# Kernel optimization log

Hardware: AMD Instinct MI355X
Metric: run time of the kernel (lower is better)

## Reference

```python
import jax, jax.numpy as jnp
import numpy as np

# Config (mirrors CorrLayerDownsample(J=3, L=8, A=1, A_prime=1, M=256, N=256,
# num_channels=1, shift_mode='samec', mask_angles=4)). With samec + 1 channel,
# every pair is 'shifted' (mask index 1) and groups (j1,j2) are contiguous in
# the global moment order, so concatenation reproduces results_storage order.
J, L, A, M, N, NB = 3, 8, 1, 256, 256, 2
MASK_ANGLES = 4
RADII = (1, 2)  # dyadic shift radii (assumed form of create_masks_shift)

def _mask_positions():
    # shift mask 1: origin plus shifts along mask_angles directions at dyadic radii
    pos = {(0, 0)}
    for k in range(MASK_ANGLES):
        th = np.pi * k / MASK_ANGLES
        for r in RADII:
            pos.add((int(round(r * np.cos(th))), int(round(r * np.sin(th)))))
    return sorted(pos)

def _union_flat_idx(h, w):
    # row-major flat indices of the union shift mask at resolution (h, w),
    # matching torch boolean-mask indexing order (mask_downsample + mask_idx_map_1)
    return np.array(sorted(((dx % h) * w + (dy % w)) for dx, dy in _mask_positions()), dtype=np.int64)

UNION_IDX = [_union_flat_idx(M >> j, N >> j) for j in range(J)]
NSHIFT = len(UNION_IDX[0])

# per-(j1,j2) channel gather indices: la = A*L*c + A*l + a = l (A=1, c=0)
# loop order in compute_idx: l1 outer, l2 inner
LA1 = np.repeat(np.arange(L), L)
LA2 = np.tile(np.arange(L), L)

def _spectral_pad(xh, Mn, Nn):
    # zero-pad Fourier representation to (Mn, Nn) -- spectral upsampling
    m, n = xh.shape[-2], xh.shape[-1]
    if (m, n) == (Mn, Nn):
        return xh
    xs = jnp.fft.fftshift(xh, axes=(-2, -1))
    ph, pw = (Mn - m) // 2, (Nn - n) // 2
    pad = [(0, 0)] * (xh.ndim - 2) + [(ph, ph), (pw, pw)]
    xp = jnp.pad(xs, pad)
    return jnp.fft.ifftshift(xp, axes=(-2, -1)) * ((Mn * Nn) / (m * n))

def _forward(xpsi_0, xpsi_1, xpsi_2):
    xs = [xpsi_0, xpsi_1, xpsi_2]
    hats = [jnp.fft.fft2(x.astype(jnp.complex64)) for x in xs]  # [nb, C, h_j, w_j]
    la1 = jnp.asarray(LA1)
    la2 = jnp.asarray(LA2)
    outs = []
    for j1 in range(J):
        h, w = M >> j1, N >> j1
        uidx = jnp.asarray(UNION_IDX[j1])
        h1 = hats[j1][:, la1]  # [nb, P=L*L, h, w]
        for j2 in range(j1, J):
            h2 = hats[j2][:, la2]
            if j2 > j1:
                h2 = _spectral_pad(h2, h, w)  # upsample coarser scale to scale j1
            corr = jnp.fft.ifft2(h1 * jnp.conj(h2)).real  # cross-correlation map
            flat = corr.reshape(corr.shape[0], corr.shape[1], h * w)
            outs.append(flat[:, :, uidx])  # masked downsample: keep shift positions
    return jnp.concatenate(outs, axis=1)  # [nb, total_pairs, NSHIFT]

def setup_inputs():
    key = jax.random.key(0)
    ks = jax.random.split(key, 3)
    return {
        "xpsi_0": jax.random.normal(ks[0], (NB, A * L, M, N), dtype=jnp.float32),
        "xpsi_1": jax.random.normal(ks[1], (NB, A * L, M // 2, N // 2), dtype=jnp.float32),
        "xpsi_2": jax.random.normal(ks[2], (NB, A * L, M // 4, N // 4), dtype=jnp.float32),
    }

def reference(xpsi_0, xpsi_1, xpsi_2):
    return _forward(xpsi_0, xpsi_1, xpsi_2)
```

## Files before the change

### kernel.cpp

```cpp
#include <hip/hip_runtime.h>

#define PI_D 3.14159265358979323846
#define PI_F 3.14159265358979323846f


__device__ inline float rtab_val(int n, int m2, int t) {
  if (t == 0) return 1.0f;
  double th = PI_D * (double)t / (double)n;
  double v = sin(th * (double)(m2 - 1)) / sin(th) + cos(th * (double)m2);
  return (float)(v / (double)m2);
}

__global__ __launch_bounds__(256) void k_front(
    const float* __restrict__ X0, const float* __restrict__ X1,
    const float* __restrict__ X2, float* __restrict__ P1p,
    float* __restrict__ P2p, float* __restrict__ V01, float* __restrict__ V02,
    float* __restrict__ V12, float* __restrict__ T01, float* __restrict__ T02,
    float* __restrict__ T12, float* __restrict__ out) {
  __shared__ float fsm[2304];
  int bid = blockIdx.x;
  int t = threadIdx.x;
  if (bid == 512) {
    for (int i = t; i < 5376; i += 256) out[i] = 0.f;
    return;
  }
  if (bid < 192) {
    const float* X; float* P; int lg, nsp, idx0;
    if (bid < 128) { X = X1; P = P1p; lg = 7; nsp = 8; idx0 = bid; }
    else           { X = X2; P = P2p; lg = 6; nsp = 4; idx0 = bid - 128; }
    int ch = idx0 / nsp, split = idx0 % nsp;
    int n = 1 << lg;
    int total = n * n;
    int chunk = total / nsp;
    int b0 = split * chunk;
    const float* x = X + (size_t)ch * total + b0;
    float s = 0.f;
    for (int i = t; i < chunk; i += 256) {
      int idx = b0 + i;
      float v = x[i];
      s += (((idx >> lg) ^ idx) & 1) ? -v : v;
    }
#pragma unroll
    for (int off = 32; off > 0; off >>= 1) s += __shfl_down(s, off, 64);
    __shared__ float red[4];
    if ((t & 63) == 0) red[t >> 6] = s;
    __syncthreads();
    if (t == 0) P[ch * nsp + split] = red[0] + red[1] + red[2] + red[3];
    return;
  }
  if (bid < 320) {
    int idx = bid - 192;
    int ch = idx >> 3, nxg = (idx & 7) * 16;
    float* Rl = fsm;
    float* Xs = fsm + 256;
    for (int i = t; i < 256; i += 256) Rl[i] = rtab_val(256, 128, i);
    const float4* xch4 =
        (const float4*)(X1 + (size_t)ch * 16384 + (size_t)nxg * 128);
    for (int i = t; i < 512; i += 256) ((float4*)Xs)[i] = xch4[i];
    __syncthreads();
    if (idx == 0)
      for (int i = t; i < 256; i += 256) T01[i] = Rl[i];
    float* vch = V01 + (size_t)ch * 128 * 256;
    for (int i = t; i < 2048; i += 256) {
      int r = i >> 7, k = i & 127;
      vch[(size_t)(nxg + r) * 256 + 2 * k] = Xs[r * 128 + k];
    }
    int cid = t & 63, wq = t >> 6;
    int m0 = 2 * cid + 1, m1 = 2 * cid + 129;
    float acc[4][2];
#pragma unroll
    for (int r = 0; r < 4; ++r) { acc[r][0] = 0.f; acc[r][1] = 0.f; }
    for (int ny = 0; ny < 128; ++ny) {
      float r0 = Rl[(m0 - 2 * ny) & 255];
      float r1 = Rl[(m1 - 2 * ny) & 255];
#pragma unroll
      for (int r = 0; r < 4; ++r) {
        float xv = Xs[(4 * wq + r) * 128 + ny];
        acc[r][0] += xv * r0;
        acc[r][1] += xv * r1;
      }
    }
#pragma unroll
    for (int r = 0; r < 4; ++r) {
      vch[(size_t)(nxg + 4 * wq + r) * 256 + m0] = acc[r][0];
      vch[(size_t)(nxg + 4 * wq + r) * 256 + m1] = acc[r][1];
    }
    return;
  }
  {
    int vbid = bid - 320;
    const float* X = X2; float* V;
    int n1, n2, s, ch, nxg, colh;
    if (vbid < 128) {
      V = V02; n1 = 256; n2 = 64; s = 4;
      ch = vbid >> 3; nxg = ((vbid >> 1) & 3) * 16; colh = vbid & 1;
    } else {
      int w = vbid - 128;
      V = V12; n1 = 128; n2 = 64; s = 2;
      ch = w >> 2; nxg = (w & 3) * 16; colh = 0;
    }
    float* Rl = fsm;
    float* Xs = fsm + 256;
    for (int i = t; i < n1; i += 256) Rl[i] = rtab_val(n1, n2, i);
    const float4* xch4 =
        (const float4*)(X + (size_t)ch * n2 * n2 + (size_t)nxg * n2);
    int nx4 = (16 * n2) >> 2;
    for (int i = t; i < nx4; i += 256) ((float4*)Xs)[i] = xch4[i];
    __syncthreads();
    if (vbid == 0)
      for (int i = t; i < 256; i += 256) T02[i] = Rl[i];
    if (vbid == 128)
      for (int i = t; i < 128; i += 256) T12[i] = Rl[i];
    int myq = (t & 63) + colh * 128;
    int nxq = t >> 6;
    int mask = n1 - 1;
    float acc[4][2];
#pragma unroll
    for (int r = 0; r < 4; ++r)
#pragma unroll
      for (int c = 0; c < 2; ++c) acc[r][c] = 0.f;
    for (int ny = 0; ny < n2; ++ny) {
      float xv[4];
#pragma unroll
      for (int r = 0; r < 4; ++r) xv[r] = Xs[(4 * nxq + r) * n2 + ny];
#pragma unroll
      for (int c = 0; c < 2; ++c) {
        float rv = Rl[(myq + 64 * c - s * ny) & mask];
#pragma unroll
        for (int r = 0; r < 4; ++r) acc[r][c] += xv[r] * rv;
      }
    }
    float* vch = V + (size_t)ch * n2 * n1;
#pragma unroll
    for (int r = 0; r < 4; ++r)
      for (int c = 0; c < 2; ++c)
        vch[(size_t)(nxg + 4 * nxq + r) * n1 + myq + 64 * c] = acc[r][c];
  }
}

__global__ __launch_bounds__(256) void k_main(const float* __restrict__ X0,
                                              const float* __restrict__ X1,
                                              const float* __restrict__ X2,
                                              const float* __restrict__ V01,
                                              const float* __restrict__ V02,
                                              const float* __restrict__ V12,
                                              const float* __restrict__ P1p,
                                              const float* __restrict__ P2p,
                                              const float* __restrict__ T01,
                                              const float* __restrict__ T02,
                                              const float* __restrict__ T12,
                                              float* __restrict__ out) {
  __shared__ float sRl[256];
  __shared__ float sh[4864];
  __shared__ float Vs[2][1024];
  int u = blockIdx.x;
  int t = threadIdx.x;
  int lane = t & 63;
  int wv = t >> 6;

  int b, l2, base, lgn1, mxg;
  const float* A1b;

  if (u < 640) {
    const float* V; const float* Pp; const float* T;
    int n1, n2, s, ch, chunk, nsp; float inv;
    if (u < 256) {
      V = V01; Pp = P1p; nsp = 8; A1b = X0; n1 = 256; n2 = 128; s = 2;
      inv = 1.f / 16384.f; ch = u >> 4; chunk = u & 15; lgn1 = 8; base = 64;
      T = T01;
    } else if (u < 512) {
      int w = u - 256;
      V = V02; Pp = P2p; nsp = 4; A1b = X0; n1 = 256; n2 = 64; s = 4;
      inv = 1.f / 4096.f; ch = w >> 4; chunk = w & 15; lgn1 = 8; base = 128;
      T = T02;
    } else {
      int w = u - 512;
      V = V12; Pp = P2p; nsp = 4; A1b = X1; n1 = 128; n2 = 64; s = 2;
      inv = 1.f / 4096.f; ch = w >> 3; chunk = w & 7; lgn1 = 7; base = 256;
      T = T12;
    }
    int mask = n1 - 1;
    for (int i = t; i < n1; i += 256) sRl[i] = T[i];
    mxg = chunk * 16;
    b = ch >> 3; l2 = ch & 7;
    const float* vch = V + (size_t)ch * n2 * n1;
    float Pv = 0.f;
    for (int i = 0; i < nsp; ++i) Pv += Pp[ch * nsp + i];
    float a = PI_F / (float)s;
    int per = 2 * s;

    if (n1 == 256) {
      if (s == 2) {
        for (int i = t; i < 640; i += 256) {
          int rl = 2 * (i >> 6), c4 = (i & 63) * 4;
          int mx = (mxg - 2 + rl) & 255;
          *(float4*)&sh[rl * 256 + c4] =
              *(const float4*)(vch + (size_t)(mx >> 1) * 256 + c4);
        }
      } else {
        for (int i = t; i < 320; i += 256) {
          int rl = 2 + 4 * (i >> 6), c4 = (i & 63) * 4;
          int mx = (mxg - 2 + rl) & 255;
          *(float4*)&sh[rl * 256 + c4] =
              *(const float4*)(vch + (size_t)(mx >> 2) * 256 + c4);
        }
      }
    } else {
      for (int i = t; i < 320; i += 256) {
        int rl = 2 * (i >> 5), c4 = (i & 31) * 4;
        int mx = (mxg - 2 + rl) & 127;
        *(float4*)&sh[rl * 128 + c4] =
            *(const float4*)(vch + (size_t)(mx >> 1) * 128 + c4);
      }
    }

    int nr, rls[4];
    if (s == 2) {
      if (wv == 0)      { nr = 3; rls[0] = 1;  rls[1] = 3;  rls[2] = 5;  rls[3] = 1; }
      else if (wv == 1) { nr = 2; rls[0] = 7;  rls[1] = 9;  rls[2] = 7;  rls[3] = 7; }
      else if (wv == 2) { nr = 2; rls[0] = 11; rls[1] = 13; rls[2] = 11; rls[3] = 11; }
      else              { nr = 2; rls[0] = 15; rls[1] = 17; rls[2] = 15; rls[3] = 15; }
    } else {
      if (wv == 0)      { nr = 4; rls[0] = 0;  rls[1] = 1;  rls[2] = 3;  rls[3] = 4; }
      else if (wv == 1) { nr = 4; rls[0] = 5;  rls[1] = 7;  rls[2] = 8;  rls[3] = 9; }
      else if (wv == 2) { nr = 3; rls[0] = 11; rls[1] = 12; rls[2] = 13; rls[3] = 11; }
      else              { nr = 3; rls[0] = 15; rls[1] = 16; rls[2] = 17; rls[3] = 15; }
    }
    int bj[4];
#pragma unroll
    for (int j = 0; j < 4; ++j) bj[j] = (mxg - 2 + rls[j]) & mask;

    const float4* vp4 = (const float4*)vch;
    if (n1 == 256) {
      int ntl = n2 >> 2;
      ((float4*)Vs[0])[t] = vp4[t];
      __syncthreads();
      float4 acc[4];
#pragma unroll
      for (int j = 0; j < 4; ++j) acc[j] = make_float4(0.f, 0.f, 0.f, 0.f);
      for (int tl = 0; tl < ntl; ++tl) {
        float4 stg;
        bool has = (tl + 1 < ntl);
        if (has) stg = vp4[(size_t)(tl + 1) * 256 + t];
        const float* Vc = Vs[tl & 1];
#pragma unroll
        for (int kk = 0; kk < 4; ++kk) {
          float4 vv = *(const float4*)&Vc[kk * 256 + 4 * lane];
          int ss = s * (4 * tl + kk);
#pragma unroll
          for (int j = 0; j < 4; ++j)
            if (j < nr) {
              float rv = sRl[(bj[j] - ss) & 255];
              acc[j].x += rv * vv.x;
              acc[j].y += rv * vv.y;
              acc[j].z += rv * vv.z;
              acc[j].w += rv * vv.w;
            }
        }
        if (has) ((float4*)Vs[(tl & 1) ^ 1])[t] = stg;
        __syncthreads();
      }
      float smy[4];
#pragma unroll
      for (int j = 0; j < 4; ++j)
        smy[j] = sinf(a * (float)((4 * lane + j) & (per - 1)));
#pragma unroll
      for (int j = 0; j < 4; ++j)
        if (j < nr) {
          float q = inv * sinf(a * (float)(bj[j] & (per - 1))) * Pv;
          float4 o = acc[j];
          o.x -= q * smy[0];
          o.y -= q * smy[1];
          o.z -= q * smy[2];
          o.w -= q * smy[3];
          *(float4*)&sh[rls[j] * 256 + 4 * lane] = o;
        }
    } else {
      if (t < 128) ((float4*)Vs[0])[t] = vp4[t];
      __syncthreads();
      float2 acc[4];
#pragma unroll
      for (int j = 0; j < 4; ++j) acc[j] = make_float2(0.f, 0.f);
      for (int tl = 0; tl < 16; ++tl) {
        float4 stg;
        bool has = (tl + 1 < 16) && (t < 128);
        if (has) stg = vp4[(size_t)(tl + 1) * 128 + t];
        const float* Vc = Vs[tl & 1];
#pragma unroll
        for (int kk = 0; kk < 4; ++kk) {
          float2 vv = *(const float2*)&Vc[kk * 128 + 2 * lane];
          int ss = 2 * (4 * tl + kk);
#pragma unroll
          for (int j = 0; j < 4; ++j)
            if (j < nr) {
              float rv = sRl[(bj[j] - ss) & 127];
              acc[j].x += rv * vv.x;
              acc[j].y += rv * vv.y;
            }
        }
        if (has) ((float4*)Vs[(tl & 1) ^ 1])[t] = stg;
        __syncthreads();
      }
      const float a2 = PI_F * 0.5f;
      float smy0 = sinf(a2 * (float)((2 * lane) & 3));
      float smy1 = sinf(a2 * (float)((2 * lane + 1) & 3));
#pragma unroll
      for (int j = 0; j < 4; ++j)
        if (j < nr) {
          float q = inv * sinf(a2 * (float)(bj[j] & 3)) * Pv;
          float2 o = acc[j];
          o.x -= q * smy0;
          o.y -= q * smy1;
          *(float2*)&sh[rls[j] * 128 + 2 * lane] = o;
        }
    }
  } else {
    int w = u - 640;
    const float* Ab; int loc, lgc;
    if (w < 256)      { loc = w;       Ab = X0; lgn1 = 8; lgc = 4; base = 0;   }
    else if (w < 384) { loc = w - 256; Ab = X1; lgn1 = 7; lgc = 3; base = 192; }
    else              { loc = w - 384; Ab = X2; lgn1 = 6; lgc = 2; base = 320; }
    int n1 = 1 << lgn1;
    int mask = n1 - 1;
    int n1sq = n1 * n1;
    int chunk = loc & ((1 << lgc) - 1);
    int bl2 = loc >> lgc;
    b = bl2 >> 3; l2 = bl2 & 7;
    A1b = Ab;
    const float* A2 = Ab + (size_t)(b * 8 + l2) * n1sq;
    mxg = chunk * 16;
    int nst = (19 * n1) >> 2;
    int l2n1 = lgn1 - 2;
    for (int i = t; i < nst; i += 256) {
      int rl = i >> l2n1;
      int c4 = (i & ((n1 >> 2) - 1)) * 4;
      int src = (mxg - 2 + rl) & mask;
      *(float4*)&sh[rl * n1 + c4] = *(const float4*)(A2 + (size_t)src * n1 + c4);
    }
  }
  __syncthreads();

  float accC[8][7];
#pragma unroll
  for (int i = 0; i < 8; ++i)
#pragma unroll
    for (int p = 0; p < 7; ++p) accC[i][p] = 0.f;
  {
    int n1 = 1 << lgn1;
    int mask = n1 - 1;
    int n1sq = n1 * n1;
    int lgtpr = lgn1 - 2;
    int tpr = 1 << lgtpr;
    int rif = 256 >> lgtpr;
    int rid = t >> lgtpr;
    int cid2 = t & (tpr - 1);
    int ty = cid2 * 4;
    int tym = (ty - 4) & mask;
    const float* A1 = A1b + (size_t)(b * 8) * n1sq;
    for (int rr = 0; rr < 16; rr += rif) {
      int ri = rr + rid;
      const float* r0 = &sh[(ri + 2) * n1];
      const float* r1 = &sh[(ri + 1) * n1];
      const float* r2 = &sh[ri * n1];
      const float* r3 = &sh[(ri + 3) * n1];
      float4 a0 = *(const float4*)(r0 + tym);
      float4 b0 = *(const float4*)(r0 + ty);
      float4 a1 = *(const float4*)(r1 + tym);
      float4 b1 = *(const float4*)(r1 + ty);
      float4 b2 = *(const float4*)(r2 + ty);
      float4 a3 = *(const float4*)(r3 + tym);
      float4 b3 = *(const float4*)(r3 + ty);
      const float* rA = A1 + (size_t)(mxg + ri) * n1 + ty;
#pragma unroll
      for (int l1 = 0; l1 < 8; ++l1) {
        float4 xv = *(const float4*)(rA + (size_t)l1 * n1sq);
        accC[l1][0] += xv.x * b0.x + xv.y * b0.y + xv.z * b0.z + xv.w * b0.w;
        accC[l1][1] += xv.x * a0.w + xv.y * b0.x + xv.z * b0.y + xv.w * b0.z;
        accC[l1][2] += xv.x * a0.z + xv.y * a0.w + xv.z * b0.x + xv.w * b0.y;
        accC[l1][3] += xv.x * b1.x + xv.y * b1.y + xv.z * b1.z + xv.w * b1.w;
        accC[l1][4] += xv.x * a1.w + xv.y * b1.x + xv.z * b1.y + xv.w * b1.z;
        accC[l1][5] += xv.x * b2.x + xv.y * b2.y + xv.z * b2.z + xv.w * b2.w;
        accC[l1][6] += xv.x * a3.w + xv.y * b3.x + xv.z * b3.y + xv.w * b3.z;
      }
    }
  }

  float* af = &accC[0][0];
#pragma unroll
  for (int j = 0; j < 56; ++j) {
    float v = af[j];
    v += __shfl_down(v, 32, 64);
    v += __shfl_down(v, 16, 64);
    af[j] = v;
  }
  __syncthreads();
  if (lane < 16) {
    float* rowp = sh + (wv * 16 + lane) * 60;
#pragma unroll
    for (int j = 0; j < 14; ++j)
      *(float4*)&rowp[4 * j] =
          make_float4(af[4 * j], af[4 * j + 1], af[4 * j + 2], af[4 * j + 3]);
  }
  __syncthreads();
  if (t < 224) {
    int v = t >> 2, q = t & 3;
    float s2 = 0.f;
#pragma unroll
    for (int i = 0; i < 16; ++i) s2 += sh[(q * 16 + i) * 60 + v];
    s2 += __shfl_down(s2, 2, 64);
    s2 += __shfl_down(s2, 1, 64);
    if (q == 0) {
      int l1o = v / 7, p = v % 7;
      atomicAdd(&out[((size_t)b * 384 + base + l1o * 8 + l2) * 7 + p], s2);
    }
  }
}

extern "C" void kernel_launch(void* const* d_in, const int* in_sizes, int n_in,
                              void* d_out, int out_size, void* d_ws, size_t ws_size,
                              hipStream_t stream) {
  const float* X0 = (const float*)d_in[0];
  const float* X1 = (const float*)d_in[1];
  const float* X2 = (const float*)d_in[2];
  float* out = (float*)d_out;
  float* ws = (float*)d_ws;

  float* V01 = ws + 2359296;
  float* V02 = ws + 2883584;
  float* V12 = ws + 3145728;
  float* P1p = ws + 3276800;
  float* P2p = ws + 3276928;
  float* T01 = ws + 3276992;
  float* T02 = ws + 3277248;
  float* T12 = ws + 3277504;

  k_front<<<513, 256, 0, stream>>>(X0, X1, X2, P1p, P2p, V01, V02, V12, T01,
                                   T02, T12, out);
  k_main<<<1088, 256, 0, stream>>>(X0, X1, X2, V01, V02, V12, P1p, P2p, T01,
                                   T02, T12, out);
}
```

Baseline: 94.93 us.

## Fuse spectral-upsample precompute into main kernel, drop intermediate V buffers

The separate front kernel that built upsampled intermediate arrays (V01/V02/V12), parity sums and interpolation tables in global workspace is removed. Each main block now computes the interpolation table, the alternating-sign sum and the column-direction upsampling itself, straight from the raw coarse inputs held in shared memory, and only a tiny zeroing kernel runs beforehand. This drops the global-memory round trip through the workspace and one heavy kernel launch. In exchange, the column interpolation and the table evaluation (double-precision sin) are repeated in every block, which adds redundant arithmetic and a longer dependent chain inside each block.

```diff
diff --git a/kernel.cpp b/kernel.cpp
--- a/kernel.cpp
+++ b/kernel.cpp
@@ -2,7 +2,6 @@
 
 #define PI_D 3.14159265358979323846
 #define PI_F 3.14159265358979323846f
-
 
 __device__ inline float rtab_val(int n, int m2, int t) {
   if (t == 0) return 1.0f;
@@ -11,308 +10,264 @@
   return (float)(v / (double)m2);
 }
 
-__global__ __launch_bounds__(256) void k_front(
-    const float* __restrict__ X0, const float* __restrict__ X1,
-    const float* __restrict__ X2, float* __restrict__ P1p,
-    float* __restrict__ P2p, float* __restrict__ V01, float* __restrict__ V02,
-    float* __restrict__ V12, float* __restrict__ T01, float* __restrict__ T02,
-    float* __restrict__ T12, float* __restrict__ out) {
-  __shared__ float fsm[2304];
-  int bid = blockIdx.x;
-  int t = threadIdx.x;
-  if (bid == 512) {
-    for (int i = t; i < 5376; i += 256) out[i] = 0.f;
-    return;
-  }
-  if (bid < 192) {
-    const float* X; float* P; int lg, nsp, idx0;
-    if (bid < 128) { X = X1; P = P1p; lg = 7; nsp = 8; idx0 = bid; }
-    else           { X = X2; P = P2p; lg = 6; nsp = 4; idx0 = bid - 128; }
-    int ch = idx0 / nsp, split = idx0 % nsp;
-    int n = 1 << lg;
-    int total = n * n;
-    int chunk = total / nsp;
-    int b0 = split * chunk;
-    const float* x = X + (size_t)ch * total + b0;
-    float s = 0.f;
-    for (int i = t; i < chunk; i += 256) {
-      int idx = b0 + i;
-      float v = x[i];
-      s += (((idx >> lg) ^ idx) & 1) ? -v : v;
-    }
-#pragma unroll
-    for (int off = 32; off > 0; off >>= 1) s += __shfl_down(s, off, 64);
-    __shared__ float red[4];
-    if ((t & 63) == 0) red[t >> 6] = s;
-    __syncthreads();
-    if (t == 0) P[ch * nsp + split] = red[0] + red[1] + red[2] + red[3];
-    return;
-  }
-  if (bid < 320) {
-    int idx = bid - 192;
-    int ch = idx >> 3, nxg = (idx & 7) * 16;
-    float* Rl = fsm;
-    float* Xs = fsm + 256;
-    for (int i = t; i < 256; i += 256) Rl[i] = rtab_val(256, 128, i);
-    const float4* xch4 =
-        (const float4*)(X1 + (size_t)ch * 16384 + (size_t)nxg * 128);
-    for (int i = t; i < 512; i += 256) ((float4*)Xs)[i] = xch4[i];
-    __syncthreads();
-    if (idx == 0)
-      for (int i = t; i < 256; i += 256) T01[i] = Rl[i];
-    float* vch = V01 + (size_t)ch * 128 * 256;
-    for (int i = t; i < 2048; i += 256) {
-      int r = i >> 7, k = i & 127;
-      vch[(size_t)(nxg + r) * 256 + 2 * k] = Xs[r * 128 + k];
-    }
-    int cid = t & 63, wq = t >> 6;
-    int m0 = 2 * cid + 1, m1 = 2 * cid + 129;
-    float acc[4][2];
-#pragma unroll
-    for (int r = 0; r < 4; ++r) { acc[r][0] = 0.f; acc[r][1] = 0.f; }
-    for (int ny = 0; ny < 128; ++ny) {
-      float r0 = Rl[(m0 - 2 * ny) & 255];
-      float r1 = Rl[(m1 - 2 * ny) & 255];
-#pragma unroll
-      for (int r = 0; r < 4; ++r) {
-        float xv = Xs[(4 * wq + r) * 128 + ny];
-        acc[r][0] += xv * r0;
-        acc[r][1] += xv * r1;
-      }
-    }
-#pragma unroll
-    for (int r = 0; r < 4; ++r) {
-      vch[(size_t)(nxg + 4 * wq + r) * 256 + m0] = acc[r][0];
-      vch[(size_t)(nxg + 4 * wq + r) * 256 + m1] = acc[r][1];
-    }
-    return;
-  }
-  {
-    int vbid = bid - 320;
-    const float* X = X2; float* V;
-    int n1, n2, s, ch, nxg, colh;
-    if (vbid < 128) {
-      V = V02; n1 = 256; n2 = 64; s = 4;
-      ch = vbid >> 3; nxg = ((vbid >> 1) & 3) * 16; colh = vbid & 1;
-    } else {
-      int w = vbid - 128;
-      V = V12; n1 = 128; n2 = 64; s = 2;
-      ch = w >> 2; nxg = (w & 3) * 16; colh = 0;
-    }
-    float* Rl = fsm;
-    float* Xs = fsm + 256;
-    for (int i = t; i < n1; i += 256) Rl[i] = rtab_val(n1, n2, i);
-    const float4* xch4 =
-        (const float4*)(X + (size_t)ch * n2 * n2 + (size_t)nxg * n2);
-    int nx4 = (16 * n2) >> 2;
-    for (int i = t; i < nx4; i += 256) ((float4*)Xs)[i] = xch4[i];
-    __syncthreads();
-    if (vbid == 0)
-      for (int i = t; i < 256; i += 256) T02[i] = Rl[i];
-    if (vbid == 128)
-      for (int i = t; i < 128; i += 256) T12[i] = Rl[i];
-    int myq = (t & 63) + colh * 128;
-    int nxq = t >> 6;
-    int mask = n1 - 1;
-    float acc[4][2];
-#pragma unroll
-    for (int r = 0; r < 4; ++r)
-#pragma unroll
-      for (int c = 0; c < 2; ++c) acc[r][c] = 0.f;
-    for (int ny = 0; ny < n2; ++ny) {
-      float xv[4];
-#pragma unroll
-      for (int r = 0; r < 4; ++r) xv[r] = Xs[(4 * nxq + r) * n2 + ny];
-#pragma unroll
-      for (int c = 0; c < 2; ++c) {
-        float rv = Rl[(myq + 64 * c - s * ny) & mask];
-#pragma unroll
-        for (int r = 0; r < 4; ++r) acc[r][c] += xv[r] * rv;
-      }
-    }
-    float* vch = V + (size_t)ch * n2 * n1;
-#pragma unroll
-    for (int r = 0; r < 4; ++r)
-      for (int c = 0; c < 2; ++c)
-        vch[(size_t)(nxg + 4 * nxq + r) * n1 + myq + 64 * c] = acc[r][c];
-  }
+__global__ __launch_bounds__(256) void k_zero(float* __restrict__ out) {
+  int i = blockIdx.x * 256 + threadIdx.x;
+  if (i < 5376) out[i] = 0.f;
 }
 
-__global__ __launch_bounds__(256) void k_main(const float* __restrict__ X0,
-                                              const float* __restrict__ X1,
-                                              const float* __restrict__ X2,
-                                              const float* __restrict__ V01,
-                                              const float* __restrict__ V02,
-                                              const float* __restrict__ V12,
-                                              const float* __restrict__ P1p,
-                                              const float* __restrict__ P2p,
-                                              const float* __restrict__ T01,
-                                              const float* __restrict__ T02,
-                                              const float* __restrict__ T12,
-                                              float* __restrict__ out) {
+__global__ __launch_bounds__(256) void k_all(const float* __restrict__ X0,
+                                             const float* __restrict__ X1,
+                                             const float* __restrict__ X2,
+                                             float* __restrict__ out) {
   __shared__ float sRl[256];
   __shared__ float sh[4864];
-  __shared__ float Vs[2][1024];
+  __shared__ float Xt[2048];
+  __shared__ float red[4];
   int u = blockIdx.x;
   int t = threadIdx.x;
-  int lane = t & 63;
-  int wv = t >> 6;
-
+  int lane = t & 63, wv = t >> 6;
   int b, l2, base, lgn1, mxg;
   const float* A1b;
 
   if (u < 640) {
-    const float* V; const float* Pp; const float* T;
-    int n1, n2, s, ch, chunk, nsp; float inv;
+    const float* Xsrc; int n1, n2, s, ch, chunk; float inv;
     if (u < 256) {
-      V = V01; Pp = P1p; nsp = 8; A1b = X0; n1 = 256; n2 = 128; s = 2;
-      inv = 1.f / 16384.f; ch = u >> 4; chunk = u & 15; lgn1 = 8; base = 64;
-      T = T01;
+      A1b = X0; lgn1 = 8; base = 64; ch = u >> 4; chunk = u & 15;
+      Xsrc = X1 + (size_t)ch * 16384; n1 = 256; n2 = 128; s = 2;
+      inv = 1.f / 16384.f;
     } else if (u < 512) {
       int w = u - 256;
-      V = V02; Pp = P2p; nsp = 4; A1b = X0; n1 = 256; n2 = 64; s = 4;
-      inv = 1.f / 4096.f; ch = w >> 4; chunk = w & 15; lgn1 = 8; base = 128;
-      T = T02;
+      A1b = X0; lgn1 = 8; base = 128; ch = w >> 4; chunk = w & 15;
+      Xsrc = X2 + (size_t)ch * 4096; n1 = 256; n2 = 64; s = 4;
+      inv = 1.f / 4096.f;
     } else {
       int w = u - 512;
-      V = V12; Pp = P2p; nsp = 4; A1b = X1; n1 = 128; n2 = 64; s = 2;
-      inv = 1.f / 4096.f; ch = w >> 3; chunk = w & 7; lgn1 = 7; base = 256;
-      T = T12;
+      A1b = X1; lgn1 = 7; base = 256; ch = w >> 3; chunk = w & 7;
+      Xsrc = X2 + (size_t)ch * 4096; n1 = 128; n2 = 64; s = 2;
+      inv = 1.f / 4096.f;
     }
     int mask = n1 - 1;
-    for (int i = t; i < n1; i += 256) sRl[i] = T[i];
-    mxg = chunk * 16;
-    b = ch >> 3; l2 = ch & 7;
-    const float* vch = V + (size_t)ch * n2 * n1;
-    float Pv = 0.f;
-    for (int i = 0; i < nsp; ++i) Pv += Pp[ch * nsp + i];
-    float a = PI_F / (float)s;
-    int per = 2 * s;
+    b = ch >> 3; l2 = ch & 7; mxg = chunk * 16;
+    for (int i = t; i < n1; i += 256) sRl[i] = rtab_val(n1, n2, i);
 
     if (n1 == 256) {
       if (s == 2) {
-        for (int i = t; i < 640; i += 256) {
-          int rl = 2 * (i >> 6), c4 = (i & 63) * 4;
+        for (int i = t; i < 1280; i += 256) {
+          int rl = 2 * (i >> 7), k = i & 127;
           int mx = (mxg - 2 + rl) & 255;
-          *(float4*)&sh[rl * 256 + c4] =
-              *(const float4*)(vch + (size_t)(mx >> 1) * 256 + c4);
+          sh[rl * 256 + 2 * k] = Xsrc[(size_t)(mx >> 1) * 128 + k];
         }
       } else {
         for (int i = t; i < 320; i += 256) {
-          int rl = 2 + 4 * (i >> 6), c4 = (i & 63) * 4;
+          int rl = 2 + 4 * (i >> 6), k = i & 63;
           int mx = (mxg - 2 + rl) & 255;
-          *(float4*)&sh[rl * 256 + c4] =
-              *(const float4*)(vch + (size_t)(mx >> 2) * 256 + c4);
+          sh[rl * 256 + 4 * k] = Xsrc[(size_t)(mx >> 2) * 64 + k];
         }
       }
     } else {
-      for (int i = t; i < 320; i += 256) {
-        int rl = 2 * (i >> 5), c4 = (i & 31) * 4;
+      for (int i = t; i < 640; i += 256) {
+        int rl = 2 * (i >> 6), k = i & 63;
         int mx = (mxg - 2 + rl) & 127;
-        *(float4*)&sh[rl * 128 + c4] =
-            *(const float4*)(vch + (size_t)(mx >> 1) * 128 + c4);
-      }
-    }
-
-    int nr, rls[4];
-    if (s == 2) {
-      if (wv == 0)      { nr = 3; rls[0] = 1;  rls[1] = 3;  rls[2] = 5;  rls[3] = 1; }
-      else if (wv == 1) { nr = 2; rls[0] = 7;  rls[1] = 9;  rls[2] = 7;  rls[3] = 7; }
-      else if (wv == 2) { nr = 2; rls[0] = 11; rls[1] = 13; rls[2] = 11; rls[3] = 11; }
-      else              { nr = 2; rls[0] = 15; rls[1] = 17; rls[2] = 15; rls[3] = 15; }
-    } else {
-      if (wv == 0)      { nr = 4; rls[0] = 0;  rls[1] = 1;  rls[2] = 3;  rls[3] = 4; }
-      else if (wv == 1) { nr = 4; rls[0] = 5;  rls[1] = 7;  rls[2] = 8;  rls[3] = 9; }
-      else if (wv == 2) { nr = 3; rls[0] = 11; rls[1] = 12; rls[2] = 13; rls[3] = 11; }
-      else              { nr = 3; rls[0] = 15; rls[1] = 16; rls[2] = 17; rls[3] = 15; }
-    }
-    int bj[4];
-#pragma unroll
-    for (int j = 0; j < 4; ++j) bj[j] = (mxg - 2 + rls[j]) & mask;
-
-    const float4* vp4 = (const float4*)vch;
-    if (n1 == 256) {
-      int ntl = n2 >> 2;
-      ((float4*)Vs[0])[t] = vp4[t];
-      __syncthreads();
-      float4 acc[4];
-#pragma unroll
-      for (int j = 0; j < 4; ++j) acc[j] = make_float4(0.f, 0.f, 0.f, 0.f);
-      for (int tl = 0; tl < ntl; ++tl) {
+        sh[rl * 128 + 2 * k] = Xsrc[(size_t)(mx >> 1) * 64 + k];
+      }
+    }
+
+    const float4* xp4 = (const float4*)Xsrc;
+    float pv = 0.f;
+
+    if (n1 == 256 && s == 2) {
+      int nr; int rls[3];
+      if (wv == 0)      { nr = 3; rls[0] = 1;  rls[1] = 3;  rls[2] = 5;  }
+      else if (wv == 1) { nr = 2; rls[0] = 7;  rls[1] = 9;  rls[2] = 7;  }
+      else if (wv == 2) { nr = 2; rls[0] = 11; rls[1] = 13; rls[2] = 11; }
+      else              { nr = 2; rls[0] = 15; rls[1] = 17; rls[2] = 15; }
+      int bj[3];
+#pragma unroll
+      for (int j = 0; j < 3; ++j) bj[j] = (mxg - 2 + rls[j]) & 255;
+      float4 v0 = xp4[t];
+      float rs = (float)(1 - 2 * ((t >> 5) & 1));
+      pv += rs * (v0.x - v0.y + v0.z - v0.w);
+      ((float4*)Xt)[t] = v0;
+      __syncthreads();
+      float2 acc[3];
+#pragma unroll
+      for (int j = 0; j < 3; ++j) acc[j] = make_float2(0.f, 0.f);
+      for (int tl = 0; tl < 16; ++tl) {
         float4 stg;
-        bool has = (tl + 1 < ntl);
-        if (has) stg = vp4[(size_t)(tl + 1) * 256 + t];
-        const float* Vc = Vs[tl & 1];
-#pragma unroll
-        for (int kk = 0; kk < 4; ++kk) {
-          float4 vv = *(const float4*)&Vc[kk * 256 + 4 * lane];
-          int ss = s * (4 * tl + kk);
-#pragma unroll
-          for (int j = 0; j < 4; ++j)
+        bool has = tl < 15;
+        if (has) stg = xp4[(size_t)(tl + 1) * 256 + t];
+        const float* Xc = &Xt[(tl & 1) * 1024];
+#pragma unroll
+        for (int kk = 0; kk < 8; ++kk) {
+          float2 vv = *(const float2*)&Xc[kk * 128 + 2 * lane];
+          int ss = 2 * (8 * tl + kk);
+#pragma unroll
+          for (int j = 0; j < 3; ++j)
             if (j < nr) {
               float rv = sRl[(bj[j] - ss) & 255];
               acc[j].x += rv * vv.x;
               acc[j].y += rv * vv.y;
-              acc[j].z += rv * vv.z;
-              acc[j].w += rv * vv.w;
             }
         }
-        if (has) ((float4*)Vs[(tl & 1) ^ 1])[t] = stg;
+        if (has) {
+          pv += rs * (stg.x - stg.y + stg.z - stg.w);
+          ((float4*)&Xt[((tl & 1) ^ 1) * 1024])[t] = stg;
+        }
         __syncthreads();
       }
-      float smy[4];
+#pragma unroll
+      for (int j = 0; j < 3; ++j)
+        if (j < nr) {
+          sh[rls[j] * 256 + 4 * lane] = acc[j].x;
+          sh[rls[j] * 256 + 4 * lane + 2] = acc[j].y;
+        }
+#pragma unroll
+      for (int off = 32; off > 0; off >>= 1) pv += __shfl_down(pv, off, 64);
+      if (lane == 0) red[wv] = pv;
+      __syncthreads();
+      float Pv = red[0] + red[1] + red[2] + red[3];
+      int c = t & 127, half = t >> 7;
+      int my = 2 * c + 1;
+      float smy = ((my & 3) == 1) ? 1.f : -1.f;
+      for (int it = 0; it < 10; ++it) {
+        int rl = 2 * it + half;
+        if (rl < 19) {
+          const float* Wr = &sh[rl * 256];
+          float sum = 0.f;
+#pragma unroll 4
+          for (int ny = 0; ny < 128; ++ny)
+            sum += sRl[(my - 2 * ny) & 255] * Wr[2 * ny];
+          int mxv = (mxg - 2 + rl) & 255;
+          if (mxv & 1) {
+            float qs = ((mxv & 3) == 1) ? 1.f : -1.f;
+            sum -= inv * qs * smy * Pv;
+          }
+          sh[rl * 256 + my] = sum;
+        }
+      }
+    } else if (n1 == 256) {
+      int nr; int rls[4];
+      if (wv == 0)      { nr = 4; rls[0] = 0;  rls[1] = 1;  rls[2] = 3;  rls[3] = 4;  }
+      else if (wv == 1) { nr = 4; rls[0] = 5;  rls[1] = 7;  rls[2] = 8;  rls[3] = 9;  }
+      else if (wv == 2) { nr = 3; rls[0] = 11; rls[1] = 12; rls[2] = 13; rls[3] = 11; }
+      else              { nr = 3; rls[0] = 15; rls[1] = 16; rls[2] = 17; rls[3] = 15; }
+      int bj[4];
+#pragma unroll
+      for (int j = 0; j < 4; ++j) bj[j] = (mxg - 2 + rls[j]) & 255;
+      float rs = (float)(1 - 2 * ((t >> 4) & 1));
+      if (t < 128) {
+        float4 v0 = xp4[t];
+        pv += rs * (v0.x - v0.y + v0.z - v0.w);
+        ((float4*)Xt)[t] = v0;
+      }
+      __syncthreads();
+      float acc[4] = {0.f, 0.f, 0.f, 0.f};
+      for (int tl = 0; tl < 8; ++tl) {
+        float4 stg;
+        bool has = (tl < 7) && (t < 128);
+        if (has) stg = xp4[(size_t)(tl + 1) * 128 + t];
+        const float* Xc = &Xt[(tl & 1) * 1024];
+#pragma unroll
+        for (int kk = 0; kk < 8; ++kk) {
+          float vv = Xc[kk * 64 + lane];
+          int ss = 4 * (8 * tl + kk);
+#pragma unroll
+          for (int j = 0; j < 4; ++j)
+            if (j < nr) acc[j] += sRl[(bj[j] - ss) & 255] * vv;
+        }
+        if (has) {
+          pv += rs * (stg.x - stg.y + stg.z - stg.w);
+          ((float4*)&Xt[((tl & 1) ^ 1) * 1024])[t] = stg;
+        }
+        __syncthreads();
+      }
 #pragma unroll
       for (int j = 0; j < 4; ++j)
-        smy[j] = sinf(a * (float)((4 * lane + j) & (per - 1)));
-#pragma unroll
-      for (int j = 0; j < 4; ++j)
-        if (j < nr) {
-          float q = inv * sinf(a * (float)(bj[j] & (per - 1))) * Pv;
-          float4 o = acc[j];
-          o.x -= q * smy[0];
-          o.y -= q * smy[1];
-          o.z -= q * smy[2];
-          o.w -= q * smy[3];
-          *(float4*)&sh[rls[j] * 256 + 4 * lane] = o;
-        }
+        if (j < nr) sh[rls[j] * 256 + 4 * lane] = acc[j];
+#pragma unroll
+      for (int off = 32; off > 0; off >>= 1) pv += __shfl_down(pv, off, 64);
+      if (lane == 0) red[wv] = pv;
+      __syncthreads();
+      float Pv = red[0] + red[1] + red[2] + red[3];
+      const float aa = PI_F * 0.25f;
+      if (t < 192) {
+        int g = t / 3, r = t - 3 * g;
+        int my = 4 * g + 1 + r;
+        float smy = sinf(aa * (float)(my & 7));
+        for (int rl = 0; rl < 19; ++rl) {
+          const float* Wr = &sh[rl * 256];
+          float sum = 0.f;
+#pragma unroll 4
+          for (int ny = 0; ny < 64; ++ny)
+            sum += sRl[(my - 4 * ny) & 255] * Wr[4 * ny];
+          int mxv = (mxg - 2 + rl) & 255;
+          if (mxv & 3) sum -= inv * sinf(aa * (float)(mxv & 7)) * smy * Pv;
+          sh[rl * 256 + my] = sum;
+        }
+      }
     } else {
-      if (t < 128) ((float4*)Vs[0])[t] = vp4[t];
-      __syncthreads();
-      float2 acc[4];
-#pragma unroll
-      for (int j = 0; j < 4; ++j) acc[j] = make_float2(0.f, 0.f);
-      for (int tl = 0; tl < 16; ++tl) {
+      int nr; int rls[3];
+      if (wv == 0)      { nr = 3; rls[0] = 1;  rls[1] = 3;  rls[2] = 5;  }
+      else if (wv == 1) { nr = 2; rls[0] = 7;  rls[1] = 9;  rls[2] = 7;  }
+      else if (wv == 2) { nr = 2; rls[0] = 11; rls[1] = 13; rls[2] = 11; }
+      else              { nr = 2; rls[0] = 15; rls[1] = 17; rls[2] = 15; }
+      int bj[3];
+#pragma unroll
+      for (int j = 0; j < 3; ++j) bj[j] = (mxg - 2 + rls[j]) & 127;
+      float rs = (float)(1 - 2 * ((t >> 4) & 1));
+      if (t < 128) {
+        float4 v0 = xp4[t];
+        pv += rs * (v0.x - v0.y + v0.z - v0.w);
+        ((float4*)Xt)[t] = v0;
+      }
+      __syncthreads();
+      float acc[3] = {0.f, 0.f, 0.f};
+      for (int tl = 0; tl < 8; ++tl) {
         float4 stg;
-        bool has = (tl + 1 < 16) && (t < 128);
-        if (has) stg = vp4[(size_t)(tl + 1) * 128 + t];
-        const float* Vc = Vs[tl & 1];
-#pragma unroll
-        for (int kk = 0; kk < 4; ++kk) {
-          float2 vv = *(const float2*)&Vc[kk * 128 + 2 * lane];
-          int ss = 2 * (4 * tl + kk);
-#pragma unroll
-          for (int j = 0; j < 4; ++j)
-            if (j < nr) {
-              float rv = sRl[(bj[j] - ss) & 127];
-              acc[j].x += rv * vv.x;
-              acc[j].y += rv * vv.y;
-            }
-        }
-        if (has) ((float4*)Vs[(tl & 1) ^ 1])[t] = stg;
+        bool has = (tl < 7) && (t < 128);
+        if (has) stg = xp4[(size_t)(tl + 1) * 128 + t];
+        const float* Xc = &Xt[(tl & 1) * 1024];
+#pragma unroll
+        for (int kk = 0; kk < 8; ++kk) {
+          float vv = Xc[kk * 64 + lane];
+          int ss = 2 * (8 * tl + kk);
+#pragma unroll
+          for (int j = 0; j < 3; ++j)
+            if (j < nr) acc[j] += sRl[(bj[j] - ss) & 127] * vv;
+        }
+        if (has) {
+          pv += rs * (stg.x - stg.y + stg.z - stg.w);
+          ((float4*)&Xt[((tl & 1) ^ 1) * 1024])[t] = stg;
+        }
         __syncthreads();
       }
-      const float a2 = PI_F * 0.5f;
-      float smy0 = sinf(a2 * (float)((2 * lane) & 3));
-      float smy1 = sinf(a2 * (float)((2 * lane + 1) & 3));
-#pragma unroll
-      for (int j = 0; j < 4; ++j)
-        if (j < nr) {
-          float q = inv * sinf(a2 * (float)(bj[j] & 3)) * Pv;
-          float2 o = acc[j];
-          o.x -= q * smy0;
-          o.y -= q * smy1;
-          *(float2*)&sh[rls[j] * 128 + 2 * lane] = o;
-        }
+#pragma unroll
+      for (int j = 0; j < 3; ++j)
+        if (j < nr) sh[rls[j] * 128 + 2 * lane] = acc[j];
+#pragma unroll
+      for (int off = 32; off > 0; off >>= 1) pv += __shfl_down(pv, off, 64);
+      if (lane == 0) red[wv] = pv;
+      __syncthreads();
+      float Pv = red[0] + red[1] + red[2] + red[3];
+      int c = t & 63, sub = t >> 6;
+      int my = 2 * c + 1;
+      float smy = ((my & 3) == 1) ? 1.f : -1.f;
+      for (int it = 0; it < 5; ++it) {
+        int rl = 4 * it + sub;
+        if (rl < 19) {
+          const float* Wr = &sh[rl * 128];
+          float sum = 0.f;
+#pragma unroll 4
+          for (int ny = 0; ny < 64; ++ny)
+            sum += sRl[(my - 2 * ny) & 127] * Wr[2 * ny];
+          int mxv = (mxg - 2 + rl) & 127;
+          if (mxv & 1) {
+            float qs = ((mxv & 3) == 1) ? 1.f : -1.f;
+            sum -= inv * qs * smy * Pv;
+          }
+          sh[rl * 128 + my] = sum;
+        }
+      }
     }
   } else {
     int w = u - 640;
@@ -327,7 +282,7 @@
     int bl2 = loc >> lgc;
     b = bl2 >> 3; l2 = bl2 & 7;
     A1b = Ab;
-    const float* A2 = Ab + (size_t)(b * 8 + l2) * n1sq;
+    const float* S = Ab + (size_t)(b * 8 + l2) * n1sq;
     mxg = chunk * 16;
     int nst = (19 * n1) >> 2;
     int l2n1 = lgn1 - 2;
@@ -335,7 +290,7 @@
       int rl = i >> l2n1;
       int c4 = (i & ((n1 >> 2) - 1)) * 4;
       int src = (mxg - 2 + rl) & mask;
-      *(float4*)&sh[rl * n1 + c4] = *(const float4*)(A2 + (size_t)src * n1 + c4);
+      *(float4*)&sh[rl * n1 + c4] = *(const float4*)(S + (size_t)src * n1 + c4);
     }
   }
   __syncthreads();
@@ -423,19 +378,7 @@
   const float* X1 = (const float*)d_in[1];
   const float* X2 = (const float*)d_in[2];
   float* out = (float*)d_out;
-  float* ws = (float*)d_ws;
-
-  float* V01 = ws + 2359296;
-  float* V02 = ws + 2883584;
-  float* V12 = ws + 3145728;
-  float* P1p = ws + 3276800;
-  float* P2p = ws + 3276928;
-  float* T01 = ws + 3276992;
-  float* T02 = ws + 3277248;
-  float* T12 = ws + 3277504;
-
-  k_front<<<513, 256, 0, stream>>>(X0, X1, X2, P1p, P2p, V01, V02, V12, T01,
-                                   T02, T12, out);
-  k_main<<<1088, 256, 0, stream>>>(X0, X1, X2, V01, V02, V12, P1p, P2p, T01,
-                                   T02, T12, out);
+
+  k_zero<<<21, 256, 0, stream>>>(out);
+  k_all<<<1088, 256, 0, stream>>>(X0, X1, X2, out);
 }
```

Measured after the change: 109.3 us. 15.2% more time.
